# Performance work log

Measured on AMD Instinct MI355X. Metric: run time of the kernel, lower is better.

Reference implementation:

```python
import jax, jax.numpy as jnp
import numpy as np
from jax.ops import segment_sum

N = 100000   # nodes
E = 1600000  # edges
D = 128      # node_feature_dim == hidden_dim
DE = 16      # edge_feature_dim
G = 512      # num_graphs
EPS = 1e-5   # BatchNorm eps


def setup_inputs() -> dict:
    key = jax.random.key(0)
    ks = jax.random.split(key, 24)
    inp = {
        "x": jax.random.normal(ks[0], (N, D), jnp.float32),
        "edge_index": jax.random.randint(ks[1], (2, E), 0, N, jnp.int64),
        "batch_idx": jnp.sort(jax.random.randint(ks[2], (N,), 0, G, jnp.int64)),
        "edge_attr": jax.random.normal(ks[3], (E, DE), jnp.float32),
        "num_graphs": G,
    }
    s = 1.0 / np.sqrt(D)
    # GCN layer 1 (D -> D) + BatchNorm1d (eval-mode running stats)
    inp["W1"] = jax.random.normal(ks[4], (D, D), jnp.float32) * s
    inp["b1"] = jnp.zeros((D,), jnp.float32)
    inp["g1"] = jax.random.uniform(ks[5], (D,), jnp.float32, 0.5, 1.5)
    inp["bt1"] = jax.random.normal(ks[6], (D,), jnp.float32) * 0.1
    inp["m1"] = jax.random.normal(ks[7], (D,), jnp.float32) * 0.1
    inp["v1"] = jax.random.uniform(ks[8], (D,), jnp.float32, 0.5, 1.5)
    # GCN layer 2
    inp["W2"] = jax.random.normal(ks[9], (D, D), jnp.float32) * s
    inp["b2"] = jnp.zeros((D,), jnp.float32)
    inp["g2"] = jax.random.uniform(ks[10], (D,), jnp.float32, 0.5, 1.5)
    inp["bt2"] = jax.random.normal(ks[11], (D,), jnp.float32) * 0.1
    inp["m2"] = jax.random.normal(ks[12], (D,), jnp.float32) * 0.1
    inp["v2"] = jax.random.uniform(ks[13], (D,), jnp.float32, 0.5, 1.5)
    # edge encoder: Linear(DE,D) -> ReLU -> Linear(D,D)
    inp["We1"] = jax.random.normal(ks[14], (DE, D), jnp.float32) / np.sqrt(DE)
    inp["be1"] = jnp.zeros((D,), jnp.float32)
    inp["We2"] = jax.random.normal(ks[15], (D, D), jnp.float32) * s
    inp["be2"] = jnp.zeros((D,), jnp.float32)
    return inp


def _gcn_conv(x, W, b, src, dst, n):
    # PyG GCNConv: add self-loops, sym norm D^-1/2 (A+I) D^-1/2, then X W + b
    xw = x @ W  # [n, out]
    loops = jnp.arange(n, dtype=src.dtype)
    s = jnp.concatenate([src, loops])
    d = jnp.concatenate([dst, loops])
    deg = segment_sum(jnp.ones_like(d, dtype=xw.dtype), d, num_segments=n)
    dinv = jnp.where(deg > 0, jax.lax.rsqrt(jnp.maximum(deg, 1.0)), 0.0)
    norm = dinv[s] * dinv[d]  # [e+n]
    msg = xw[s] * norm[:, None]
    return segment_sum(msg, d, num_segments=n) + b


def _bn_relu(x, g, bt, m, v):
    return jax.nn.relu((x - m) * jax.lax.rsqrt(v + EPS) * g + bt)


def reference(x, edge_index, batch_idx, edge_attr, num_graphs,
              W1, b1, g1, bt1, m1, v1,
              W2, b2, g2, bt2, m2, v2,
              We1, be1, We2, be2):
    n = x.shape[0]
    src, dst = edge_index[0], edge_index[1]
    # two GraphConvLayer: GCNConv -> BN(eval) -> ReLU -> Dropout(eval=id)
    h = _bn_relu(_gcn_conv(x, W1, b1, src, dst, n), g1, bt1, m1, v1)
    h = _bn_relu(_gcn_conv(h, W2, b2, src, dst, n), g2, bt2, m2, v2)
    # global mean pool over nodes per graph
    nsum = segment_sum(h, batch_idx, num_segments=num_graphs)
    ncnt = segment_sum(jnp.ones((n,), h.dtype), batch_idx, num_segments=num_graphs)
    graph_repr = nsum / jnp.maximum(ncnt, 1.0)[:, None]
    # edge encoder + per-graph edge mean (fused segment-mean)
    e = jax.nn.relu(edge_attr @ We1 + be1) @ We2 + be2  # [E, D]
    edge_batch = batch_idx[src]
    esum = segment_sum(e, edge_batch, num_segments=num_graphs)
    ecnt = segment_sum(jnp.ones((e.shape[0],), e.dtype), edge_batch, num_segments=num_graphs)
    edge_repr = jnp.where(ecnt[:, None] > 0, esum / jnp.maximum(ecnt, 1.0)[:, None], 0.0)
    return graph_repr + edge_repr
```

## Files before the change

### kernel.cpp

```cpp
#include <hip/hip_runtime.h>

#define N_NODES 100000
#define N_EDGES 1600000
#define D 128
#define DE 16
#define G 512
#define EPSBN 1e-5f
#define ESLICE 4
#define EPB 2048
#define EPT (EPB / 256)
#define SCHUNK 1024
#define NSB ((N_NODES + SCHUNK - 1) / SCHUNK)
#define AGG_CH 16
#define DSHIFT 9
#define DBSZ 512
#define NBKT ((N_NODES + DBSZ - 1) / DBSZ)

typedef __bf16 bf16x8 __attribute__((ext_vector_type(8)));
typedef __bf16 bf16x4 __attribute__((ext_vector_type(4)));
typedef float f32x4 __attribute__((ext_vector_type(4)));

__device__ __forceinline__ float bf_lo(unsigned v) { return __uint_as_float(v << 16); }
__device__ __forceinline__ float bf_hi(unsigned v) { return __uint_as_float(v & 0xffff0000u); }

__global__ void k_init(int* __restrict__ deg, int* __restrict__ ecnt, int* __restrict__ dcnt,
                       float* __restrict__ gcnt, float* __restrict__ gsum,
                       float* __restrict__ esum) {
  int i = blockIdx.x * 256 + threadIdx.x;
  if (i < N_NODES) deg[i] = 1;
  if (i < G) { ecnt[i] = 0; gcnt[i] = 0.f; }
  if (i < NBKT) dcnt[i] = 0;
  if (i < G * D) { gsum[i] = 0.f; esum[i] = 0.f; }
}

__global__ void k_count(const int* __restrict__ ei, const int* __restrict__ batch,
                        int* __restrict__ deg, int* __restrict__ ecnt, int* __restrict__ dcnt) {
  __shared__ int bins[G];
  __shared__ int dbins[NBKT];
  int tid = threadIdx.x;
  for (int i = tid; i < G; i += 256) bins[i] = 0;
  for (int i = tid; i < NBKT; i += 256) dbins[i] = 0;
  __syncthreads();
  int base = blockIdx.x * 4096;
  for (int t = tid; t < 4096; t += 256) {
    int e = base + t;
    if (e < N_EDGES) {
      int s = ei[e];
      int d = ei[N_EDGES + e];
      atomicAdd(&deg[d], 1);
      atomicAdd(&bins[batch[s]], 1);
      atomicAdd(&dbins[d >> DSHIFT], 1);
    }
  }
  __syncthreads();
  for (int i = tid; i < G; i += 256) if (bins[i]) atomicAdd(&ecnt[i], bins[i]);
  for (int i = tid; i < NBKT; i += 256) if (dbins[i]) atomicAdd(&dcnt[i], dbins[i]);
}

__global__ __launch_bounds__(256) void k_scan_part(const int* __restrict__ deg,
                                                   int* __restrict__ part) {
  __shared__ int red[4];
  int tid = threadIdx.x;
  int base = blockIdx.x * SCHUNK + tid * 4;
  int s = 0;
  #pragma unroll
  for (int k = 0; k < 4; ++k) {
    int i = base + k;
    if (i < N_NODES) s += deg[i];
  }
  #pragma unroll
  for (int off = 32; off > 0; off >>= 1) s += __shfl_down(s, off);
  if ((tid & 63) == 0) red[tid >> 6] = s;
  __syncthreads();
  if (tid == 0) part[blockIdx.x] = red[0] + red[1] + red[2] + red[3];
}

__global__ void k_scan_mid(int* __restrict__ part, const int* __restrict__ ecnt,
                           int* __restrict__ ebs, int* __restrict__ ecur_pad,
                           const int* __restrict__ dcnt, int* __restrict__ dbs,
                           int* __restrict__ dcur_pad) {
  __shared__ int sb[512];
  int tid = threadIdx.x;
  int v = (tid < NSB) ? part[tid] : 0;
  sb[tid] = v;
  __syncthreads();
  for (int off = 1; off < 512; off <<= 1) {
    int t = (tid >= off) ? sb[tid - off] : 0;
    __syncthreads();
    sb[tid] += t;
    __syncthreads();
  }
  if (tid < NSB) part[tid] = sb[tid] - v;
  __syncthreads();
  int v2 = ecnt[tid];
  sb[tid] = v2;
  __syncthreads();
  for (int off = 1; off < 512; off <<= 1) {
    int t = (tid >= off) ? sb[tid - off] : 0;
    __syncthreads();
    sb[tid] += t;
    __syncthreads();
  }
  ebs[tid] = sb[tid] - v2;
  ecur_pad[tid * 16] = sb[tid] - v2;
  __syncthreads();
  int v3 = (tid < NBKT) ? dcnt[tid] : 0;
  sb[tid] = v3;
  __syncthreads();
  for (int off = 1; off < 512; off <<= 1) {
    int t = (tid >= off) ? sb[tid - off] : 0;
    __syncthreads();
    sb[tid] += t;
    __syncthreads();
  }
  if (tid < NBKT) { dbs[tid] = sb[tid] - v3; dcur_pad[tid * 16] = sb[tid] - v3; }
}

__global__ __launch_bounds__(256) void k_scan_write(const int* __restrict__ deg,
                                                    const int* __restrict__ part,
                                                    int* __restrict__ rs,
                                                    float* __restrict__ dinv) {
  __shared__ int sb[256];
  int tid = threadIdx.x;
  int base = blockIdx.x * SCHUNK + tid * 4;
  int d[4];
  int s = 0;
  #pragma unroll
  for (int k = 0; k < 4; ++k) {
    int i = base + k;
    d[k] = (i < N_NODES) ? deg[i] : 0;
    s += d[k];
  }
  sb[tid] = s;
  __syncthreads();
  for (int off = 1; off < 256; off <<= 1) {
    int t = (tid >= off) ? sb[tid - off] : 0;
    __syncthreads();
    sb[tid] += t;
    __syncthreads();
  }
  int ex = sb[tid] - s + part[blockIdx.x];
  #pragma unroll
  for (int k = 0; k < 4; ++k) {
    int i = base + k;
    if (i < N_NODES) {
      rs[i] = ex;
      dinv[i] = rsqrtf((float)d[k]);
      ex += d[k];
    }
  }
}

__global__ __launch_bounds__(256) void k_scatter(const int* __restrict__ ei,
                                                 const int* __restrict__ batch,
                                                 const float* __restrict__ edge_attr,
                                                 int* __restrict__ ecur_pad,
                                                 int* __restrict__ dcur_pad,
                                                 int2* __restrict__ pairs,
                                                 __bf16* __restrict__ eaS) {
  __shared__ int gbins[G];
  __shared__ int gbase[G];
  __shared__ int dbins[NBKT];
  __shared__ int dbase[NBKT];
  __shared__ int gsrc[EPB];
  __shared__ int gdst[EPB];
  __shared__ int dsrc[EPB];
  __shared__ int ddst[EPB];
  int tid = threadIdx.x;
  for (int i = tid; i < G; i += 256) gbins[i] = 0;
  for (int i = tid; i < NBKT; i += 256) dbins[i] = 0;
  __syncthreads();
  int e0 = blockIdx.x * EPB;
  int nvalid = N_EDGES - e0;
  if (nvalid > EPB) nvalid = EPB;
  int ge[EPT], gr[EPT], db[EPT], dr[EPT];
  #pragma unroll
  for (int k = 0; k < EPT; ++k) {
    int e = e0 + k * 256 + tid;
    ge[k] = -1;
    if (e < N_EDGES) {
      int s = ei[e], d = ei[N_EDGES + e];
      int g = batch[s];
      ge[k] = g;
      gr[k] = atomicAdd(&gbins[g], 1);
      db[k] = d >> DSHIFT;
      dr[k] = atomicAdd(&dbins[db[k]], 1);
    }
  }
  __syncthreads();
  for (int i = tid; i < G; i += 256) {
    int cnt = gbins[i];
    gbase[i] = cnt ? atomicAdd(&ecur_pad[i * 16], cnt) : 0;
  }
  for (int i = tid; i < NBKT; i += 256) {
    int cnt = dbins[i];
    dbase[i] = cnt ? atomicAdd(&dcur_pad[i * 16], cnt) : 0;
  }
  int v0 = gbins[tid], v1 = gbins[tid + 256];
  int vd = (tid < NBKT) ? dbins[tid] : 0;
  gsrc[tid] = vd;
  __syncthreads();
  for (int off = 1; off < 512; off <<= 1) {
    int a = (tid >= off) ? gbins[tid - off] : 0;
    int b = gbins[tid + 256 - off];
    int c = (off < 256 && tid >= off) ? gsrc[tid - off] : 0;
    __syncthreads();
    gbins[tid] += a;
    gbins[tid + 256] += b;
    if (off < 256) gsrc[tid] += c;
    __syncthreads();
  }
  gbins[tid] -= v0;
  gbins[tid + 256] -= v1;
  if (tid < NBKT) dbins[tid] = gsrc[tid] - vd;
  __syncthreads();
  #pragma unroll
  for (int k = 0; k < EPT; ++k) {
    if (ge[k] >= 0) {
      int e = e0 + k * 256 + tid;
      int g = ge[k];
      int sG = gbins[g] + gr[k];
      gsrc[sG] = e;
      gdst[sG] = gbase[g] + gr[k];
      int bkt = db[k];
      int sD = dbins[bkt] + dr[k];
      dsrc[sD] = e;
      ddst[sD] = dbase[bkt] + dr[k];
    }
  }
  __syncthreads();
  for (int p = tid; p < nvalid; p += 256) {
    int e = gsrc[p];
    int dst = gdst[p];
    const float4* q = (const float4*)(edge_attr + (size_t)e * DE);
    float4 f0 = q[0], f1 = q[1], f2 = q[2], f3 = q[3];
    bf16x8 h0, h1;
    h0[0] = (__bf16)f0.x; h0[1] = (__bf16)f0.y; h0[2] = (__bf16)f0.z; h0[3] = (__bf16)f0.w;
    h0[4] = (__bf16)f1.x; h0[5] = (__bf16)f1.y; h0[6] = (__bf16)f1.z; h0[7] = (__bf16)f1.w;
    h1[0] = (__bf16)f2.x; h1[1] = (__bf16)f2.y; h1[2] = (__bf16)f2.z; h1[3] = (__bf16)f2.w;
    h1[4] = (__bf16)f3.x; h1[5] = (__bf16)f3.y; h1[6] = (__bf16)f3.z; h1[7] = (__bf16)f3.w;
    bf16x8* w = (bf16x8*)(eaS + (size_t)dst * DE);
    w[0] = h0; w[1] = h1;
  }
  for (int p = tid; p < nvalid; p += 256) {
    int e = dsrc[p];
    int s = ei[e], d = ei[N_EDGES + e];
    pairs[ddst[p]] = make_int2(s, d);
  }
}

__global__ __launch_bounds__(256) void k_scatter_nbr(const int2* __restrict__ pairs,
                                                     const int* __restrict__ dbs,
                                                     const int* __restrict__ dcnt,
                                                     const int* __restrict__ rs,
                                                     int* __restrict__ nbr) {
  __shared__ int cur[DBSZ];
  int tid = threadIdx.x;
  int bkt = blockIdx.x;
  int nodeBase = bkt << DSHIFT;
  for (int l = tid; l < DBSZ; l += 256) {
    int node = nodeBase + l;
    cur[l] = (node < N_NODES) ? rs[node] : 0;
  }
  __syncthreads();
  int start = dbs[bkt], n = dcnt[bkt];
  for (int i = tid; i < n; i += 256) {
    int2 p = pairs[start + i];
    int pos = atomicAdd(&cur[p.y - nodeBase], 1);
    nbr[pos] = p.x;
  }
}

__global__ void k_prep_w(const float* __restrict__ W, __bf16* __restrict__ Wf) {
  int tid = threadIdx.x;
  for (int idx = blockIdx.x * 256 + tid; idx < 16384; idx += 8 * 256) {
    int j = idx & 7;
    int lane = (idx >> 3) & 63;
    int cb = (idx >> 9) & 7;
    int kc = idx >> 12;
    int k = kc * 32 + (lane >> 4) * 8 + j;
    int n = cb * 16 + (lane & 15);
    Wf[idx] = (__bf16)W[k * 128 + n];
  }
}

__global__ __launch_bounds__(256) void k_gemm_mfma(const float* __restrict__ X,
                                                   const __bf16* __restrict__ Wf,
                                                   const float* __restrict__ dinv,
                                                   __bf16* __restrict__ out) {
  __shared__ __bf16 sXb[64][136];
  int tid = threadIdx.x;
  int wave = tid >> 6, lane = tid & 63;
  int m = lane & 15, kg = lane >> 4;
  int base = blockIdx.x * 64;
  #pragma unroll
  for (int i = 0; i < 8; ++i) {
    int idx = tid + i * 256;
    int r = idx >> 5, cq = idx & 31;
    int row = base + r;
    float4 v = make_float4(0.f, 0.f, 0.f, 0.f);
    if (row < N_NODES) v = *(const float4*)(X + (size_t)row * 128 + cq * 4);
    bf16x4 h;
    h[0] = (__bf16)v.x; h[1] = (__bf16)v.y; h[2] = (__bf16)v.z; h[3] = (__bf16)v.w;
    *(bf16x4*)(&sXb[r][cq * 4]) = h;
  }
  __syncthreads();
  int r0 = wave * 16;
  f32x4 acc[8];
  #pragma unroll
  for (int cb = 0; cb < 8; ++cb) acc[cb] = (f32x4){0.f, 0.f, 0.f, 0.f};
  #pragma unroll
  for (int kc = 0; kc < 4; ++kc) {
    bf16x8 afrag = *(const bf16x8*)(&sXb[r0 + m][kc * 32 + kg * 8]);
    #pragma unroll
    for (int cb = 0; cb < 8; ++cb) {
      bf16x8 bfrag = *(const bf16x8*)(Wf + (((size_t)(kc * 8 + cb) * 64 + lane) << 3));
      acc[cb] = __builtin_amdgcn_mfma_f32_16x16x32_bf16(afrag, bfrag, acc[cb], 0, 0, 0);
    }
  }
  #pragma unroll
  for (int r = 0; r < 4; ++r) {
    int grow = base + r0 + kg * 4 + r;
    if (grow < N_NODES) {
      float dv = dinv[grow];
      #pragma unroll
      for (int cb = 0; cb < 8; ++cb)
        out[(size_t)grow * 128 + cb * 16 + m] = (__bf16)(acc[cb][r] * dv);
    }
  }
}

__global__ __launch_bounds__(256) void k_agg_bn(const unsigned* __restrict__ Au,
                                                const int* __restrict__ nbr,
                                                const int* __restrict__ rs,
                                                const int* __restrict__ deg,
                                                const float* __restrict__ dinv,
                                                const float* __restrict__ b,
                                                const float* __restrict__ gm,
                                                const float* __restrict__ bt,
                                                const float* __restrict__ m,
                                                const float* __restrict__ v,
                                                float* __restrict__ outB) {
  int tid = threadIdx.x;
  int wave = tid >> 6, lane = tid & 63;
  int c0 = lane * 2, c1 = c0 + 1;
  float sc0 = gm[c0] * rsqrtf(v[c0] + EPSBN), sc1 = gm[c1] * rsqrtf(v[c1] + EPSBN);
  float sh0 = bt[c0] - m[c0] * sc0, sh1 = bt[c1] - m[c1] * sc1;
  float bb0 = b[c0], bb1 = b[c1];
  int base = (blockIdx.x * 4 + wave) * AGG_CH;
  for (int nn = 0; nn < AGG_CH; ++nn) {
    int i = base + nn;
    if (i >= N_NODES) return;
    unsigned sv = Au[(size_t)i * 64 + lane];
    float s0 = bf_lo(sv), s1 = bf_hi(sv);
    int j = rs[i];
    int end = j + deg[i] - 1;
    for (; j + 3 < end; j += 4) {
      int n0 = nbr[j], n1 = nbr[j + 1], n2 = nbr[j + 2], n3 = nbr[j + 3];
      unsigned a0 = Au[(size_t)n0 * 64 + lane];
      unsigned a1 = Au[(size_t)n1 * 64 + lane];
      unsigned a2 = Au[(size_t)n2 * 64 + lane];
      unsigned a3 = Au[(size_t)n3 * 64 + lane];
      s0 += bf_lo(a0) + bf_lo(a1) + bf_lo(a2) + bf_lo(a3);
      s1 += bf_hi(a0) + bf_hi(a1) + bf_hi(a2) + bf_hi(a3);
    }
    for (; j < end; ++j) {
      unsigned a = Au[(size_t)nbr[j] * 64 + lane];
      s0 += bf_lo(a); s1 += bf_hi(a);
    }
    float dv = dinv[i];
    float y0 = fmaxf((dv * s0 + bb0) * sc0 + sh0, 0.f);
    float y1 = fmaxf((dv * s1 + bb1) * sc1 + sh1, 0.f);
    *(float2*)(outB + (size_t)i * 128 + c0) = make_float2(y0, y1);
  }
}

__global__ __launch_bounds__(256) void k_agg_bn_pool(const unsigned* __restrict__ Au,
                                                     const int* __restrict__ nbr,
                                                     const int* __restrict__ rs,
                                                     const int* __restrict__ deg,
                                                     const float* __restrict__ dinv,
                                                     const int* __restrict__ batch,
                                                     const float* __restrict__ b,
                                                     const float* __restrict__ gm,
                                                     const float* __restrict__ bt,
                                                     const float* __restrict__ m,
                                                     const float* __restrict__ v,
                                                     float* __restrict__ gsum,
                                                     float* __restrict__ gcnt) {
  int tid = threadIdx.x;
  int wave = tid >> 6, lane = tid & 63;
  int c0 = lane * 2, c1 = c0 + 1;
  float sc0 = gm[c0] * rsqrtf(v[c0] + EPSBN), sc1 = gm[c1] * rsqrtf(v[c1] + EPSBN);
  float sh0 = bt[c0] - m[c0] * sc0, sh1 = bt[c1] - m[c1] * sc1;
  float bb0 = b[c0], bb1 = b[c1];
  int base = (blockIdx.x * 4 + wave) * AGG_CH;
  if (base >= N_NODES) return;
  float acc0 = 0.f, acc1 = 0.f, cnt = 0.f;
  int curg = -1;
  for (int nn = 0; nn < AGG_CH; ++nn) {
    int i = base + nn;
    if (i >= N_NODES) break;
    int bg = batch[i];
    if (bg != curg) {
      if (curg >= 0) {
        atomicAdd(&gsum[(size_t)curg * 128 + c0], acc0);
        atomicAdd(&gsum[(size_t)curg * 128 + c1], acc1);
        if (lane == 0) atomicAdd(&gcnt[curg], cnt);
      }
      acc0 = 0.f; acc1 = 0.f; cnt = 0.f; curg = bg;
    }
    unsigned sv = Au[(size_t)i * 64 + lane];
    float s0 = bf_lo(sv), s1 = bf_hi(sv);
    int j = rs[i];
    int end = j + deg[i] - 1;
    for (; j + 3 < end; j += 4) {
      int n0 = nbr[j], n1 = nbr[j + 1], n2 = nbr[j + 2], n3 = nbr[j + 3];
      unsigned a0 = Au[(size_t)n0 * 64 + lane];
      unsigned a1 = Au[(size_t)n1 * 64 + lane];
      unsigned a2 = Au[(size_t)n2 * 64 + lane];
      unsigned a3 = Au[(size_t)n3 * 64 + lane];
      s0 += bf_lo(a0) + bf_lo(a1) + bf_lo(a2) + bf_lo(a3);
      s1 += bf_hi(a0) + bf_hi(a1) + bf_hi(a2) + bf_hi(a3);
    }
    for (; j < end; ++j) {
      unsigned a = Au[(size_t)nbr[j] * 64 + lane];
      s0 += bf_lo(a); s1 += bf_hi(a);
    }
    float dv = dinv[i];
    acc0 += fmaxf((dv * s0 + bb0) * sc0 + sh0, 0.f);
    acc1 += fmaxf((dv * s1 + bb1) * sc1 + sh1, 0.f);
    cnt += 1.f;
  }
  if (curg >= 0) {
    atomicAdd(&gsum[(size_t)curg * 128 + c0], acc0);
    atomicAdd(&gsum[(size_t)curg * 128 + c1], acc1);
    if (lane == 0) atomicAdd(&gcnt[curg], cnt);
  }
}

__global__ __launch_bounds__(256) void k_edge_hidden(
    const __bf16* __restrict__ eaS,
    const int* __restrict__ ebs, const int* __restrict__ ecnt,
    const float* __restrict__ We1, const float* __restrict__ be1,
    float* __restrict__ esum) {
  int tid = threadIdx.x;
  int wave = tid >> 6;
  int lane = tid & 63;
  int n = lane & 15;
  int kg = lane >> 4;
  int g = blockIdx.x / ESLICE;
  int slice = blockIdx.x % ESLICE;

  bf16x8 bfrag[8];
  float biasv[8];
  #pragma unroll
  for (int blk = 0; blk < 8; ++blk) {
    #pragma unroll
    for (int j = 0; j < 8; ++j) {
      int k = kg * 8 + j;
      float w = (k < DE) ? We1[k * 128 + blk * 16 + n] : 0.f;
      bfrag[blk][j] = (__bf16)w;
    }
    biasv[blk] = be1[blk * 16 + n];
  }

  int start = ebs[g], cnt = ecnt[g];
  int lim = start + cnt;
  int ntiles = (cnt + 15) >> 4;
  const int nstream = ESLICE * 4;
  int sid = slice * 4 + wave;
  int tpc = (ntiles + nstream - 1) / nstream;
  int t0 = sid * tpc;
  int t1 = t0 + tpc; if (t1 > ntiles) t1 = ntiles;

  float racc[8] = {0.f, 0.f, 0.f, 0.f, 0.f, 0.f, 0.f, 0.f};

  for (int t = t0; t < t1; ++t) {
    int jb = start + (t << 4);
    int row = jb + n;
    int rc = row < lim - 1 ? row : lim - 1;
    bf16x8 afrag = {};
    if (kg < 2) afrag = *(const bf16x8*)(eaS + (size_t)rc * DE + kg * 8);
    bool full = (jb + 16 <= lim);
    if (full) {
      #pragma unroll
      for (int blk = 0; blk < 8; ++blk) {
        f32x4 acc = {0.f, 0.f, 0.f, 0.f};
        acc = __builtin_amdgcn_mfma_f32_16x16x32_bf16(afrag, bfrag[blk], acc, 0, 0, 0);
        #pragma unroll
        for (int r = 0; r < 4; ++r)
          racc[blk] += fmaxf(acc[r] + biasv[blk], 0.f);
      }
    } else {
      #pragma unroll
      for (int blk = 0; blk < 8; ++blk) {
        f32x4 acc = {0.f, 0.f, 0.f, 0.f};
        acc = __builtin_amdgcn_mfma_f32_16x16x32_bf16(afrag, bfrag[blk], acc, 0, 0, 0);
        #pragma unroll
        for (int r = 0; r < 4; ++r) {
          int rr = kg * 4 + r;
          if (jb + rr < lim) racc[blk] += fmaxf(acc[r] + biasv[blk], 0.f);
        }
      }
    }
  }

  #pragma unroll
  for (int blk = 0; blk < 8; ++blk) {
    float vsum = racc[blk];
    vsum += __shfl_xor(vsum, 16);
    vsum += __shfl_xor(vsum, 32);
    if (lane < 16) atomicAdd(&esum[(size_t)g * 128 + blk * 16 + n], vsum);
  }
}

__global__ void k_final(const float* __restrict__ esum, const int* __restrict__ ecnt,
                        const float* __restrict__ gsum, const float* __restrict__ gcnt,
                        const float* __restrict__ We2, const float* __restrict__ be2,
                        float* __restrict__ out) {
  __shared__ float mh[128];
  int g = blockIdx.x, c = threadIdx.x;
  int ec = ecnt[g];
  mh[c] = (ec > 0) ? esum[(size_t)g * 128 + c] / (float)ec : 0.f;
  __syncthreads();
  float acc = 0.f;
  #pragma unroll 8
  for (int k = 0; k < 128; ++k) acc += mh[k] * We2[k * 128 + c];
  float er = (ec > 0) ? (acc + be2[c]) : 0.f;
  float gr = gsum[(size_t)g * 128 + c] / fmaxf(gcnt[g], 1.f);
  out[(size_t)g * 128 + c] = gr + er;
}

extern "C" void kernel_launch(void* const* d_in, const int* in_sizes, int n_in,
                              void* d_out, int out_size, void* d_ws, size_t ws_size,
                              hipStream_t stream) {
  const float* x        = (const float*)d_in[0];
  const int*   ei       = (const int*)d_in[1];
  const int*   batch    = (const int*)d_in[2];
  const float* edge_attr= (const float*)d_in[3];
  const float* W1 = (const float*)d_in[5];
  const float* b1 = (const float*)d_in[6];
  const float* g1 = (const float*)d_in[7];
  const float* bt1= (const float*)d_in[8];
  const float* m1 = (const float*)d_in[9];
  const float* v1 = (const float*)d_in[10];
  const float* W2 = (const float*)d_in[11];
  const float* b2 = (const float*)d_in[12];
  const float* g2 = (const float*)d_in[13];
  const float* bt2= (const float*)d_in[14];
  const float* m2 = (const float*)d_in[15];
  const float* v2 = (const float*)d_in[16];
  const float* We1= (const float*)d_in[17];
  const float* be1= (const float*)d_in[18];
  const float* We2= (const float*)d_in[19];
  const float* be2= (const float*)d_in[20];
  float* out = (float*)d_out;

  char* ws = (char*)d_ws;
  size_t off = 0;
  auto take = [&](size_t bytes) -> char* {
    char* p = ws + off;
    off += (bytes + 255) & ~(size_t)255;
    return p;
  };
  __bf16* A       = (__bf16*)take((size_t)N_NODES * 128 * 2);
  float*  B       = (float*) take((size_t)N_NODES * 128 * 4);
  float*  dinv    = (float*) take((size_t)N_NODES * 4);
  int*    deg     = (int*)   take((size_t)N_NODES * 4);
  int*    rs      = (int*)   take((size_t)N_NODES * 4);
  int*    nbr     = (int*)   take((size_t)(N_EDGES + N_NODES) * 4);
  int2*   pairs   = (int2*)  take((size_t)N_EDGES * 8);
  __bf16* eaS     = (__bf16*)take((size_t)N_EDGES * DE * 2);
  __bf16* Wf1     = (__bf16*)take((size_t)16384 * 2);
  __bf16* Wf2     = (__bf16*)take((size_t)16384 * 2);
  int*    ecnt    = (int*)   take((size_t)G * 4);
  int*    ebs     = (int*)   take((size_t)G * 4);
  int*    ecur_pad= (int*)   take((size_t)G * 16 * 4);
  int*    dcnt    = (int*)   take((size_t)NBKT * 4);
  int*    dbs     = (int*)   take((size_t)NBKT * 4);
  int*    dcur_pad= (int*)   take((size_t)NBKT * 16 * 4);
  float*  gcnt    = (float*) take((size_t)G * 4);
  float*  esum    = (float*) take((size_t)G * 128 * 4);
  float*  gsum    = (float*) take((size_t)G * 128 * 4);
  int*    part    = (int*)   take((size_t)NSB * 4);

  k_init<<<(N_NODES + 255) / 256, 256, 0, stream>>>(deg, ecnt, dcnt, gcnt, gsum, esum);
  k_prep_w<<<8, 256, 0, stream>>>(W1, Wf1);
  k_prep_w<<<8, 256, 0, stream>>>(W2, Wf2);
  k_count<<<(N_EDGES + 4095) / 4096, 256, 0, stream>>>(ei, batch, deg, ecnt, dcnt);
  k_scan_part<<<NSB, 256, 0, stream>>>(deg, part);
  k_scan_mid<<<1, 512, 0, stream>>>(part, ecnt, ebs, ecur_pad, dcnt, dbs, dcur_pad);
  k_scan_write<<<NSB, 256, 0, stream>>>(deg, part, rs, dinv);
  k_scatter<<<(N_EDGES + EPB - 1) / EPB, 256, 0, stream>>>(ei, batch, edge_attr, ecur_pad, dcur_pad, pairs, eaS);
  k_scatter_nbr<<<NBKT, 256, 0, stream>>>(pairs, dbs, dcnt, rs, nbr);
  const int aggBlocks = (N_NODES + 4 * AGG_CH - 1) / (4 * AGG_CH);
  k_gemm_mfma<<<(N_NODES + 63) / 64, 256, 0, stream>>>(x, Wf1, dinv, A);
  k_agg_bn<<<aggBlocks, 256, 0, stream>>>((const unsigned*)A, nbr, rs, deg, dinv, b1, g1, bt1, m1, v1, B);
  k_gemm_mfma<<<(N_NODES + 63) / 64, 256, 0, stream>>>(B, Wf2, dinv, A);
  k_agg_bn_pool<<<aggBlocks, 256, 0, stream>>>((const unsigned*)A, nbr, rs, deg, dinv, batch, b2, g2, bt2, m2, v2, gsum, gcnt);
  k_edge_hidden<<<G * ESLICE, 256, 0, stream>>>(eaS, ebs, ecnt, We1, be1, esum);
  k_final<<<G, 128, 0, stream>>>(esum, ecnt, gsum, gcnt, We2, be2, out);
}
```

Measured before the change: 716.8 us.

## Scatter edge indices instead of bf16 edge features; gather attributes in edge encoder

The scatter kernel no longer reads edge_attr and writes a graph-sorted bf16 copy. It now writes only a permutation list of edge ids, and the edge-hidden kernel gathers the fp32 attributes through that list and converts them to bf16 when it loads them. The edges-per-block count is also halved, which gives more scatter blocks with smaller shared-memory footprints. This removes a 51 MB intermediate write and read, but makes the encoder's loads indirect, 64-byte rows from random locations.

```diff
diff --git a/kernel.cpp b/kernel.cpp
--- a/kernel.cpp
+++ b/kernel.cpp
@@ -7,7 +7,7 @@
 #define G 512
 #define EPSBN 1e-5f
 #define ESLICE 4
-#define EPB 2048
+#define EPB 1024
 #define EPT (EPB / 256)
 #define SCHUNK 1024
 #define NSB ((N_NODES + SCHUNK - 1) / SCHUNK)
@@ -153,11 +153,10 @@
 
 __global__ __launch_bounds__(256) void k_scatter(const int* __restrict__ ei,
                                                  const int* __restrict__ batch,
-                                                 const float* __restrict__ edge_attr,
                                                  int* __restrict__ ecur_pad,
                                                  int* __restrict__ dcur_pad,
                                                  int2* __restrict__ pairs,
-                                                 __bf16* __restrict__ eaS) {
+                                                 int* __restrict__ idlist) {
   __shared__ int gbins[G];
   __shared__ int gbase[G];
   __shared__ int dbins[NBKT];
@@ -217,35 +216,24 @@
   #pragma unroll
   for (int k = 0; k < EPT; ++k) {
     if (ge[k] >= 0) {
-      int e = e0 + k * 256 + tid;
+      int el = k * 256 + tid;
       int g = ge[k];
       int sG = gbins[g] + gr[k];
-      gsrc[sG] = e;
+      gsrc[sG] = el;
       gdst[sG] = gbase[g] + gr[k];
       int bkt = db[k];
       int sD = dbins[bkt] + dr[k];
-      dsrc[sD] = e;
+      dsrc[sD] = el;
       ddst[sD] = dbase[bkt] + dr[k];
     }
   }
   __syncthreads();
   for (int p = tid; p < nvalid; p += 256) {
-    int e = gsrc[p];
-    int dst = gdst[p];
-    const float4* q = (const float4*)(edge_attr + (size_t)e * DE);
-    float4 f0 = q[0], f1 = q[1], f2 = q[2], f3 = q[3];
-    bf16x8 h0, h1;
-    h0[0] = (__bf16)f0.x; h0[1] = (__bf16)f0.y; h0[2] = (__bf16)f0.z; h0[3] = (__bf16)f0.w;
-    h0[4] = (__bf16)f1.x; h0[5] = (__bf16)f1.y; h0[6] = (__bf16)f1.z; h0[7] = (__bf16)f1.w;
-    h1[0] = (__bf16)f2.x; h1[1] = (__bf16)f2.y; h1[2] = (__bf16)f2.z; h1[3] = (__bf16)f2.w;
-    h1[4] = (__bf16)f3.x; h1[5] = (__bf16)f3.y; h1[6] = (__bf16)f3.z; h1[7] = (__bf16)f3.w;
-    bf16x8* w = (bf16x8*)(eaS + (size_t)dst * DE);
-    w[0] = h0; w[1] = h1;
+    idlist[gdst[p]] = e0 + gsrc[p];
   }
   for (int p = tid; p < nvalid; p += 256) {
-    int e = dsrc[p];
-    int s = ei[e], d = ei[N_EDGES + e];
-    pairs[ddst[p]] = make_int2(s, d);
+    int e = e0 + dsrc[p];
+    pairs[ddst[p]] = make_int2(ei[e], ei[N_EDGES + e]);
   }
 }
 
@@ -440,7 +428,8 @@
 }
 
 __global__ __launch_bounds__(256) void k_edge_hidden(
-    const __bf16* __restrict__ eaS,
+    const float* __restrict__ edge_attr,
+    const int* __restrict__ idlist,
     const int* __restrict__ ebs, const int* __restrict__ ecnt,
     const float* __restrict__ We1, const float* __restrict__ be1,
     float* __restrict__ esum) {
@@ -481,7 +470,15 @@
     int row = jb + n;
     int rc = row < lim - 1 ? row : lim - 1;
     bf16x8 afrag = {};
-    if (kg < 2) afrag = *(const bf16x8*)(eaS + (size_t)rc * DE + kg * 8);
+    if (kg < 2) {
+      int e = idlist[rc];
+      const float4* q = (const float4*)(edge_attr + (size_t)e * DE + kg * 8);
+      float4 f0 = q[0], f1 = q[1];
+      afrag[0] = (__bf16)f0.x; afrag[1] = (__bf16)f0.y;
+      afrag[2] = (__bf16)f0.z; afrag[3] = (__bf16)f0.w;
+      afrag[4] = (__bf16)f1.x; afrag[5] = (__bf16)f1.y;
+      afrag[6] = (__bf16)f1.z; afrag[7] = (__bf16)f1.w;
+    }
     bool full = (jb + 16 <= lim);
     if (full) {
       #pragma unroll
@@ -571,7 +568,7 @@
   int*    rs      = (int*)   take((size_t)N_NODES * 4);
   int*    nbr     = (int*)   take((size_t)(N_EDGES + N_NODES) * 4);
   int2*   pairs   = (int2*)  take((size_t)N_EDGES * 8);
-  __bf16* eaS     = (__bf16*)take((size_t)N_EDGES * DE * 2);
+  int*    idlist  = (int*)   take((size_t)N_EDGES * 4);
   __bf16* Wf1     = (__bf16*)take((size_t)16384 * 2);
   __bf16* Wf2     = (__bf16*)take((size_t)16384 * 2);
   int*    ecnt    = (int*)   take((size_t)G * 4);
@@ -592,13 +589,13 @@
   k_scan_part<<<NSB, 256, 0, stream>>>(deg, part);
   k_scan_mid<<<1, 512, 0, stream>>>(part, ecnt, ebs, ecur_pad, dcnt, dbs, dcur_pad);
   k_scan_write<<<NSB, 256, 0, stream>>>(deg, part, rs, dinv);
-  k_scatter<<<(N_EDGES + EPB - 1) / EPB, 256, 0, stream>>>(ei, batch, edge_attr, ecur_pad, dcur_pad, pairs, eaS);
+  k_scatter<<<(N_EDGES + EPB - 1) / EPB, 256, 0, stream>>>(ei, batch, ecur_pad, dcur_pad, pairs, idlist);
   k_scatter_nbr<<<NBKT, 256, 0, stream>>>(pairs, dbs, dcnt, rs, nbr);
   const int aggBlocks = (N_NODES + 4 * AGG_CH - 1) / (4 * AGG_CH);
   k_gemm_mfma<<<(N_NODES + 63) / 64, 256, 0, stream>>>(x, Wf1, dinv, A);
   k_agg_bn<<<aggBlocks, 256, 0, stream>>>((const unsigned*)A, nbr, rs, deg, dinv, b1, g1, bt1, m1, v1, B);
   k_gemm_mfma<<<(N_NODES + 63) / 64, 256, 0, stream>>>(B, Wf2, dinv, A);
   k_agg_bn_pool<<<aggBlocks, 256, 0, stream>>>((const unsigned*)A, nbr, rs, deg, dinv, batch, b2, g2, bt2, m2, v2, gsum, gcnt);
-  k_edge_hidden<<<G * ESLICE, 256, 0, stream>>>(eaS, ebs, ecnt, We1, be1, esum);
+  k_edge_hidden<<<G * ESLICE, 256, 0, stream>>>(edge_attr, idlist, ebs, ecnt, We1, be1, esum);
   k_final<<<G, 128, 0, stream>>>(esum, ecnt, gsum, gcnt, We2, be2, out);
 }
```

After: 697.7 us. 1.03x faster.
